# Optimization experiments

Measured on AMD Instinct MI355X. Metric: run time of the kernel, lower is better.

The kernel has to match this reference:

```python
import jax, jax.numpy as jnp
import numpy as np

EPS = 1e-5
ROPE_BASE = 10000.0

def rms_norm(x, w):
    return x * jax.lax.rsqrt(jnp.mean(x * x, axis=-1, keepdims=True) + EPS) * w

def rope_cos_sin(positions, head_dim):
    inv_freq = 1.0 / (ROPE_BASE ** (jnp.arange(0, head_dim, 2, dtype=jnp.float32) / head_dim))
    ang = positions.astype(jnp.float32)[:, None] * inv_freq[None, :]          # [L, hd/2]
    emb = jnp.concatenate([ang, ang], axis=-1)                                # [L, hd]
    return jnp.cos(emb), jnp.sin(emb)

def rotate_half(x):
    d = x.shape[-1] // 2
    return jnp.concatenate([-x[..., d:], x[..., :d]], axis=-1)

def apply_rope(x, cos, sin):
    # x: [B,H,L,hd]; cos/sin: [L,hd]
    return x * cos[None, None] + rotate_half(x) * sin[None, None]

def setup_inputs() -> dict:
    key = jax.random.key(0)
    ks = jax.random.split(key, 12)
    B, S, D = 1, 2048, 2048
    H, KVH, HD = 16, 8, 128
    FF, CACHE = 5632, 2048
    s = 0.02
    return {
        "hidden_states": jax.random.normal(ks[0], (B, S, D), jnp.float32),
        "k_cache": jax.random.normal(ks[1], (B, H, CACHE, HD), jnp.float32),
        "v_cache": jax.random.normal(ks[2], (B, H, CACHE, HD), jnp.float32),
        "q_w": jax.random.normal(ks[3], (H * HD, D), jnp.float32) * s,
        "k_w": jax.random.normal(ks[4], (KVH * HD, D), jnp.float32) * s,
        "v_w": jax.random.normal(ks[5], (KVH * HD, D), jnp.float32) * s,
        "o_w": jax.random.normal(ks[6], (D, H * HD), jnp.float32) * s,
        "gate_w": jax.random.normal(ks[7], (FF, D), jnp.float32) * s,
        "up_w": jax.random.normal(ks[8], (FF, D), jnp.float32) * s,
        "down_w": jax.random.normal(ks[9], (D, FF), jnp.float32) * s,
        "ln1_w": jnp.ones((D,), jnp.float32),
        "ln2_w": jnp.ones((D,), jnp.float32),
        "chunk_size": 512,
    }

def reference(hidden_states, k_cache, v_cache, q_w, k_w, v_w, o_w,
              gate_w, up_w, down_w, ln1_w, ln2_w, chunk_size):
    B, S, D = hidden_states.shape
    H = k_cache.shape[1]
    HD = k_cache.shape[-1]
    KVH = k_w.shape[0] // HD
    group = H // KVH
    prefix = k_cache.shape[2]

    # --- input RMSNorm ---
    residual = hidden_states
    h = rms_norm(hidden_states, ln1_w)

    # --- QKV projections (GQA) ---
    q = (h @ q_w.T).reshape(B, S, H, HD).transpose(0, 2, 1, 3)                # [B,H,S,hd]
    k = (h @ k_w.T).reshape(B, S, KVH, HD).transpose(0, 2, 1, 3)              # [B,KVH,S,hd]
    v = (h @ v_w.T).reshape(B, S, KVH, HD).transpose(0, 2, 1, 3)
    k = jnp.repeat(k, group, axis=1)                                          # repeat_kv -> [B,H,S,hd]
    v = jnp.repeat(v, group, axis=1)

    # --- KV-cache concat along seq ---
    keys = jnp.concatenate([k_cache, k], axis=2)                              # [B,H,P+S,hd]
    vals = jnp.concatenate([v_cache, v], axis=2)
    kv_len = prefix + S

    # --- inline RoPE: keys at 0..kv_len-1, queries at prefix..kv_len-1 ---
    cos_k, sin_k = rope_cos_sin(jnp.arange(kv_len), HD)
    q = apply_rope(q, cos_k[prefix:], sin_k[prefix:])
    keys = apply_rope(keys, cos_k, sin_k)

    # --- hybrid chunked attention mask ---
    # query i (local) sees: full cache prefix + causal positions within its own chunk
    i = jnp.arange(S)
    j = jnp.arange(kv_len)
    local_j = j - prefix
    prefix_vis = (j[None, :] < prefix)
    same_chunk = (i[:, None] // chunk_size) == (local_j[None, :] // chunk_size)
    causal = local_j[None, :] <= i[:, None]
    mask = prefix_vis | (same_chunk & causal)                                 # [S, kv_len]

    scores = jnp.einsum("bhqd,bhkd->bhqk", q, keys) / jnp.sqrt(jnp.float32(HD))
    scores = jnp.where(mask[None, None], scores, jnp.finfo(scores.dtype).min)
    probs = jax.nn.softmax(scores, axis=-1)
    attn = jnp.einsum("bhqk,bhkd->bhqd", probs, vals)                         # [B,H,S,hd]
    attn = attn.transpose(0, 2, 1, 3).reshape(B, S, H * HD) @ o_w.T

    h = residual + attn

    # --- SwiGLU MLP ---
    residual = h
    h = rms_norm(h, ln2_w)
    h = (jax.nn.silu(h @ gate_w.T) * (h @ up_w.T)) @ down_w.T
    return residual + h
```

## Files before the change

### kernel.cpp

```cpp
#include <hip/hip_runtime.h>


#define S_LEN   2048
#define D_MODEL 2048
#define NH      16
#define KVHEADS 8
#define HDIM    128
#define FFDIM   5632
#define PREFIX  2048
#define KVLEN   4096
#define SM_SCALE 0.08838834764831845f
#define LN10K_64 0.14391156831212787f

using bf16x8 = __attribute__((ext_vector_type(8))) short;
using f32x4  = __attribute__((ext_vector_type(4))) float;

__device__ __forceinline__ unsigned f2bf_u(float f) {
  unsigned u = __float_as_uint(f);
  return (u + 0x7fffu + ((u >> 16) & 1u)) >> 16;
}
__device__ __forceinline__ unsigned short f2bf(float f) { return (unsigned short)f2bf_u(f); }
__device__ __forceinline__ float bf2f(unsigned short u) {
  return __uint_as_float((unsigned)u << 16);
}
__device__ __forceinline__ uint2 pack4(float4 v) {
  uint2 r;
  r.x = f2bf_u(v.x) | (f2bf_u(v.y) << 16);
  r.y = f2bf_u(v.z) | (f2bf_u(v.w) << 16);
  return r;
}
__device__ __forceinline__ f32x4 mfma16(bf16x8 a, bf16x8 b, f32x4 c) {
  return __builtin_amdgcn_mfma_f32_16x16x32_bf16(a, b, c, 0, 0, 0);
}
__device__ __forceinline__ void gl2lds16(const unsigned short* g, unsigned short* l) {
  __builtin_amdgcn_global_load_lds(
      (__attribute__((address_space(1))) void*)(unsigned short*)g,
      (__attribute__((address_space(3))) void*)l, 16, 0, 0);
}

__global__ __launch_bounds__(256) void convw_k(const float* __restrict__ src,
                                               unsigned short* __restrict__ dst) {
  size_t i = (size_t)blockIdx.x * 256 + threadIdx.x;
  const float4* s4 = (const float4*)src;
  float4 a = s4[2 * i], b = s4[2 * i + 1];
  uint2 lo = pack4(a), hi = pack4(b);
  ((uint4*)dst)[i] = make_uint4(lo.x, lo.y, hi.x, hi.y);
}

template <bool INBF>
__global__ __launch_bounds__(256) void rmsnorm_k(const void* __restrict__ xin,
                                                 const float* __restrict__ w,
                                                 unsigned short* __restrict__ out) {
  const int row = blockIdx.x, tid = threadIdx.x;
  float v[8];
  if constexpr (INBF) {
    const unsigned short* xr = (const unsigned short*)xin + (size_t)row * D_MODEL;
    uint4 u = ((const uint4*)xr)[tid];
    v[0] = bf2f((unsigned short)(u.x & 0xffff)); v[1] = bf2f((unsigned short)(u.x >> 16));
    v[2] = bf2f((unsigned short)(u.y & 0xffff)); v[3] = bf2f((unsigned short)(u.y >> 16));
    v[4] = bf2f((unsigned short)(u.z & 0xffff)); v[5] = bf2f((unsigned short)(u.z >> 16));
    v[6] = bf2f((unsigned short)(u.w & 0xffff)); v[7] = bf2f((unsigned short)(u.w >> 16));
  } else {
    const float4* xr = (const float4*)((const float*)xin + (size_t)row * D_MODEL);
    float4 a = xr[2 * tid], b = xr[2 * tid + 1];
    v[0] = a.x; v[1] = a.y; v[2] = a.z; v[3] = a.w;
    v[4] = b.x; v[5] = b.y; v[6] = b.z; v[7] = b.w;
  }
  float ss = 0.f;
#pragma unroll
  for (int i = 0; i < 8; i++) ss += v[i] * v[i];
#pragma unroll
  for (int off = 1; off < 64; off <<= 1) ss += __shfl_xor(ss, off);
  __shared__ float red[4];
  if ((tid & 63) == 0) red[tid >> 6] = ss;
  __syncthreads();
  const float sc = rsqrtf((red[0] + red[1] + red[2] + red[3]) * (1.0f / D_MODEL) + 1e-5f);
  const float4* w4 = (const float4*)w;
  float4 wa = w4[2 * tid], wb = w4[2 * tid + 1];
  float4 oa = make_float4(v[0]*sc*wa.x, v[1]*sc*wa.y, v[2]*sc*wa.z, v[3]*sc*wa.w);
  float4 ob = make_float4(v[4]*sc*wb.x, v[5]*sc*wb.y, v[6]*sc*wb.z, v[7]*sc*wb.w);
  uint2 lo = pack4(oa), hi = pack4(ob);
  ((uint4*)(out + (size_t)row * D_MODEL))[tid] = make_uint4(lo.x, lo.y, hi.x, hi.y);
}

template <int BN, int EPI>
__global__ __launch_bounds__(256) void gemm_bf(const unsigned short* __restrict__ A,
                                               const unsigned short* __restrict__ B,
                                               const void* __restrict__ res,
                                               void* __restrict__ C,
                                               int M, int N, int K) {
  constexpr int NI = BN / 32;
  __shared__ __align__(16) unsigned short lA[128 * 32];
  __shared__ __align__(16) unsigned short lB[BN * 32];
  const int tid = threadIdx.x, lane = tid & 63, wave = tid >> 6;
  const int r16 = lane & 15, q4 = lane >> 4;
  const int wm = wave >> 1, wn = wave & 1;
  const int m0 = blockIdx.x * 128, n0 = blockIdx.y * BN;

  const int lr = lane >> 2;
  const int lc = (lane & 3) * 8;
  const unsigned short* gA0 = A + (size_t)(m0 + wave * 16 + lr) * K + lc;
  const unsigned short* gA1 = A + (size_t)(m0 + 64 + wave * 16 + lr) * K + lc;
  unsigned short* lA0 = lA + (wave * 16) * 32;
  unsigned short* lA1 = lA + (64 + wave * 16) * 32;
  const unsigned short* gB0 = B + (size_t)(n0 + wave * 16 + lr) * K + lc;
  const unsigned short* gB1 = B + (size_t)(n0 + 64 + wave * 16 + lr) * K + lc;
  unsigned short* lB0 = lB + (wave * 16) * 32;
  unsigned short* lB1 = lB + (64 + wave * 16) * 32;

  f32x4 acc[4][NI];
#pragma unroll
  for (int i = 0; i < 4; i++)
#pragma unroll
    for (int j = 0; j < NI; j++) acc[i][j] = f32x4{0.f, 0.f, 0.f, 0.f};

  for (int k0 = 0; k0 < K; k0 += 32) {
    gl2lds16(gA0, lA0);
    gl2lds16(gA1, lA1);
    gl2lds16(gB0, lB0);
    if constexpr (BN == 128) gl2lds16(gB1, lB1);
    gA0 += 32; gA1 += 32; gB0 += 32;
    if constexpr (BN == 128) gB1 += 32;
    __syncthreads();
    bf16x8 af[4], bfr[NI];
#pragma unroll
    for (int mi = 0; mi < 4; mi++)
      af[mi] = *(const bf16x8*)&lA[(wm * 64 + mi * 16 + r16) * 32 + q4 * 8];
#pragma unroll
    for (int ni = 0; ni < NI; ni++)
      bfr[ni] = *(const bf16x8*)&lB[(wn * (BN / 2) + ni * 16 + r16) * 32 + q4 * 8];
#pragma unroll
    for (int mi = 0; mi < 4; mi++)
#pragma unroll
      for (int ni = 0; ni < NI; ni++)
        acc[mi][ni] = mfma16(af[mi], bfr[ni], acc[mi][ni]);
    __syncthreads();
  }
#pragma unroll
  for (int mi = 0; mi < 4; mi++)
#pragma unroll
    for (int ni = 0; ni < NI; ni++) {
      int col = n0 + wn * (BN / 2) + ni * 16 + r16;
#pragma unroll
      for (int rr = 0; rr < 4; rr++) {
        int row = m0 + wm * 64 + mi * 16 + q4 * 4 + rr;
        size_t idx = (size_t)row * N + col;
        float v = acc[mi][ni][rr];
        if constexpr (EPI == 0) {
          ((unsigned short*)C)[idx] = f2bf(v);
        } else if constexpr (EPI == 1) {
          ((unsigned short*)C)[idx] = f2bf(v + ((const float*)res)[idx]);
        } else {
          ((float*)C)[idx] = v + bf2f(((const unsigned short*)res)[idx]);
        }
      }
    }
}

__global__ __launch_bounds__(256) void gemm_gateup(const unsigned short* __restrict__ A,
                                                   const unsigned short* __restrict__ Bg,
                                                   const unsigned short* __restrict__ Bu,
                                                   unsigned short* __restrict__ act) {
  __shared__ __align__(16) unsigned short lA[128 * 32];
  __shared__ __align__(16) unsigned short lG[64 * 32];
  __shared__ __align__(16) unsigned short lU[64 * 32];
  const int tid = threadIdx.x, lane = tid & 63, wave = tid >> 6;
  const int r16 = lane & 15, q4 = lane >> 4;
  const int wm = wave >> 1, wn = wave & 1;
  const int m0 = blockIdx.x * 128, n0 = blockIdx.y * 64;
  const int K = D_MODEL;

  const int lr = lane >> 2, lc = (lane & 3) * 8;
  const unsigned short* gA0 = A + (size_t)(m0 + wave * 16 + lr) * K + lc;
  const unsigned short* gA1 = A + (size_t)(m0 + 64 + wave * 16 + lr) * K + lc;
  unsigned short* lA0 = lA + (wave * 16) * 32;
  unsigned short* lA1 = lA + (64 + wave * 16) * 32;
  const unsigned short* gG0 = Bg + (size_t)(n0 + wave * 16 + lr) * K + lc;
  const unsigned short* gU0 = Bu + (size_t)(n0 + wave * 16 + lr) * K + lc;
  unsigned short* lG0 = lG + (wave * 16) * 32;
  unsigned short* lU0 = lU + (wave * 16) * 32;

  f32x4 ag[4][2], au[4][2];
#pragma unroll
  for (int i = 0; i < 4; i++)
#pragma unroll
    for (int j = 0; j < 2; j++) { ag[i][j] = f32x4{0.f,0.f,0.f,0.f}; au[i][j] = f32x4{0.f,0.f,0.f,0.f}; }

  for (int k0 = 0; k0 < K; k0 += 32) {
    gl2lds16(gA0, lA0);
    gl2lds16(gA1, lA1);
    gl2lds16(gG0, lG0);
    gl2lds16(gU0, lU0);
    gA0 += 32; gA1 += 32; gG0 += 32; gU0 += 32;
    __syncthreads();
    bf16x8 af[4], bg2[2], bu2[2];
#pragma unroll
    for (int mi = 0; mi < 4; mi++)
      af[mi] = *(const bf16x8*)&lA[(wm * 64 + mi * 16 + r16) * 32 + q4 * 8];
#pragma unroll
    for (int ni = 0; ni < 2; ni++) {
      int r = (wn * 32 + ni * 16 + r16) * 32 + q4 * 8;
      bg2[ni] = *(const bf16x8*)&lG[r];
      bu2[ni] = *(const bf16x8*)&lU[r];
    }
#pragma unroll
    for (int mi = 0; mi < 4; mi++)
#pragma unroll
      for (int ni = 0; ni < 2; ni++) {
        ag[mi][ni] = mfma16(af[mi], bg2[ni], ag[mi][ni]);
        au[mi][ni] = mfma16(af[mi], bu2[ni], au[mi][ni]);
      }
    __syncthreads();
  }
#pragma unroll
  for (int mi = 0; mi < 4; mi++)
#pragma unroll
    for (int ni = 0; ni < 2; ni++) {
      int col = n0 + wn * 32 + ni * 16 + r16;
#pragma unroll
      for (int rr = 0; rr < 4; rr++) {
        int row = m0 + wm * 64 + mi * 16 + q4 * 4 + rr;
        float g = ag[mi][ni][rr], u = au[mi][ni][rr];
        float sil = g / (1.0f + __expf(-g));
        act[(size_t)row * FFDIM + col] = f2bf(sil * u);
      }
    }
}

__global__ __launch_bounds__(256) void rope_q_k(const unsigned short* __restrict__ qkv,
                                                unsigned short* __restrict__ q_bf) {
  int idx = blockIdx.x * 256 + threadIdx.x;
  int d = idx & 127, s = (idx >> 7) & 2047, h = idx >> 18;
  int dd = d & 63;
  float inv = __expf(-(float)dd * LN10K_64);
  float ang = (float)(PREFIX + s) * inv;
  float c = cosf(ang), sn = sinf(ang);
  const unsigned short* row = qkv + (size_t)s * 4096 + h * HDIM;
  float x = bf2f(row[d]);
  float xr = (d < 64) ? -bf2f(row[d + 64]) : bf2f(row[d - 64]);
  q_bf[idx] = f2bf(x * c + xr * sn);
}

__global__ __launch_bounds__(256) void rope_k_k(const float* __restrict__ k_cache,
                                                const unsigned short* __restrict__ qkv,
                                                unsigned short* __restrict__ keys_bf) {
  int idx = blockIdx.x * 256 + threadIdx.x;
  int d = idx & 127, j = (idx >> 7) & 4095, h = idx >> 19;
  int dd = d & 63;
  float inv = __expf(-(float)dd * LN10K_64);
  float ang = (float)j * inv;
  float c = cosf(ang), sn = sinf(ang);
  float x, xr;
  if (j < PREFIX) {
    const float* row = k_cache + ((size_t)h * PREFIX + j) * HDIM;
    x = row[d];
    xr = (d < 64) ? -row[d + 64] : row[d - 64];
  } else {
    const unsigned short* row = qkv + (size_t)(j - PREFIX) * 4096 + 2048 + (h >> 1) * HDIM;
    x = bf2f(row[d]);
    xr = (d < 64) ? -bf2f(row[d + 64]) : bf2f(row[d - 64]);
  }
  keys_bf[idx] = f2bf(x * c + xr * sn);
}

__global__ __launch_bounds__(256) void vtrans_k(const float* __restrict__ v_cache,
                                                const unsigned short* __restrict__ qkv,
                                                unsigned short* __restrict__ vals_t) {
  __shared__ float tile[32][33];
  const int h = blockIdx.z, j0 = blockIdx.x * 32, d0 = blockIdx.y * 32;
  const int t = threadIdx.x;
#pragma unroll
  for (int i = 0; i < 4; i++) {
    int e = i * 256 + t;
    int jj = e >> 5, dd = e & 31;
    float v;
    if (j0 < PREFIX)
      v = v_cache[((size_t)h * PREFIX + j0 + jj) * HDIM + d0 + dd];
    else
      v = bf2f(qkv[(size_t)(j0 - PREFIX + jj) * 4096 + 3072 + (h >> 1) * HDIM + d0 + dd]);
    tile[jj][dd] = v;
  }
  __syncthreads();
#pragma unroll
  for (int i = 0; i < 4; i++) {
    int e = i * 256 + t;
    int dd = e >> 5, jj = e & 31;
    vals_t[((size_t)h * HDIM + d0 + dd) * KVLEN + j0 + jj] = f2bf(tile[jj][dd]);
  }
}

__global__ __launch_bounds__(256) void attn_k(const unsigned short* __restrict__ qbf,
                                              const unsigned short* __restrict__ keys,
                                              const unsigned short* __restrict__ valst,
                                              const int* __restrict__ chunkp,
                                              unsigned short* __restrict__ out) {
  __shared__ uint4 ldsK[512];
  __shared__ uint4 ldsV[512];
  __shared__ __align__(16) unsigned short ldsP[4][512];
  const int h = blockIdx.y, q0 = blockIdx.x * 64;
  const int tid = threadIdx.x, wave = tid >> 6, lane = tid & 63;
  const int r16 = lane & 15, q4 = lane >> 4;
  const int chunk = chunkp[0];

  bf16x8 qf[4];
  const unsigned short* qrow = qbf + ((size_t)h * S_LEN + q0 + wave * 16 + r16) * HDIM + q4 * 8;
#pragma unroll
  for (int ks = 0; ks < 4; ks++) qf[ks] = *(const bf16x8*)(qrow + ks * 32);

  float mrow[4], lrow[4];
  f32x4 oacc[8];
#pragma unroll
  for (int rr = 0; rr < 4; rr++) { mrow[rr] = -1e30f; lrow[rr] = 0.f; }
#pragma unroll
  for (int ni = 0; ni < 8; ni++) oacc[ni] = f32x4{0.f, 0.f, 0.f, 0.f};

  const int irow_base = q0 + wave * 16 + q4 * 4;

  auto tile_step = [&](int kglob, int jloc0, bool domask) {
#pragma unroll
    for (int i = 0; i < 2; i++) {
      int gid = i * 256 + tid;
      int kk = gid >> 4, c8 = gid & 15;
      uint4 v = *(const uint4*)(keys + ((size_t)h * KVLEN + kglob + kk) * HDIM + c8 * 8);
      int ks = c8 >> 2, q8 = c8 & 3;
      ldsK[((ks * 2 + (kk >> 4)) << 6) + (q8 << 4) + ((kk & 15) ^ (q8 << 1))] = v;
    }
#pragma unroll
    for (int i = 0; i < 2; i++) {
      int gid = i * 256 + tid;
      int n = gid >> 2, c8 = gid & 3;
      uint4 v = *(const uint4*)(valst + ((size_t)h * HDIM + n) * KVLEN + kglob + c8 * 8);
      ldsV[((n >> 4) << 6) + (c8 << 4) + ((n & 15) ^ (c8 << 1))] = v;
    }
    __syncthreads();
    f32x4 s0{0.f,0.f,0.f,0.f}, s1{0.f,0.f,0.f,0.f};
#pragma unroll
    for (int ks = 0; ks < 4; ks++) {
      bf16x8 k0f = *(const bf16x8*)&ldsK[((ks * 2 + 0) << 6) + (q4 << 4) + (r16 ^ (q4 << 1))];
      bf16x8 k1f = *(const bf16x8*)&ldsK[((ks * 2 + 1) << 6) + (q4 << 4) + (r16 ^ (q4 << 1))];
      s0 = mfma16(qf[ks], k0f, s0);
      s1 = mfma16(qf[ks], k1f, s1);
    }
    float al[4];
#pragma unroll
    for (int rr = 0; rr < 4; rr++) {
      float a = s0[rr] * SM_SCALE, b = s1[rr] * SM_SCALE;
      if (domask) {
        int irow = irow_base + rr;
        if (jloc0 + r16 > irow)       a = -1e30f;
        if (jloc0 + 16 + r16 > irow)  b = -1e30f;
      }
      float mx = fmaxf(a, b);
      mx = fmaxf(mx, __shfl_xor(mx, 1));
      mx = fmaxf(mx, __shfl_xor(mx, 2));
      mx = fmaxf(mx, __shfl_xor(mx, 4));
      mx = fmaxf(mx, __shfl_xor(mx, 8));
      float mn = fmaxf(mrow[rr], mx);
      float alpha = __expf(mrow[rr] - mn);
      mrow[rr] = mn;
      a = __expf(a - mn); b = __expf(b - mn);
      float sum = a + b;
      sum += __shfl_xor(sum, 1); sum += __shfl_xor(sum, 2);
      sum += __shfl_xor(sum, 4); sum += __shfl_xor(sum, 8);
      lrow[rr] = lrow[rr] * alpha + sum;
      al[rr] = alpha;
      int rowi = q4 * 4 + rr;
      ldsP[wave][((r16 >> 3) * 16 + rowi) * 8 + (r16 & 7)] = f2bf(a);
      ldsP[wave][(((r16 >> 3) + 2) * 16 + rowi) * 8 + (r16 & 7)] = f2bf(b);
    }
#pragma unroll
    for (int ni = 0; ni < 8; ni++) {
      oacc[ni][0] *= al[0]; oacc[ni][1] *= al[1];
      oacc[ni][2] *= al[2]; oacc[ni][3] *= al[3];
    }
    __syncthreads();
    bf16x8 pf = *(const bf16x8*)&ldsP[wave][lane * 8];
#pragma unroll
    for (int ni = 0; ni < 8; ni++) {
      bf16x8 vf = *(const bf16x8*)&ldsV[(ni << 6) + (q4 << 4) + (r16 ^ (q4 << 1))];
      oacc[ni] = mfma16(pf, vf, oacc[ni]);
    }
    __syncthreads();
  };

  for (int kb = 0; kb < PREFIX; kb += 32) tile_step(kb, 0, false);
  const int cs = (q0 / chunk) * chunk;
  for (int lkb = cs; lkb < q0 + 64; lkb += 32) tile_step(PREFIX + lkb, lkb, true);

#pragma unroll
  for (int ni = 0; ni < 8; ni++)
#pragma unroll
    for (int rr = 0; rr < 4; rr++) {
      int q = irow_base + rr;
      int dcol = ni * 16 + r16;
      out[(size_t)q * D_MODEL + h * HDIM + dcol] = f2bf(oacc[ni][rr] / lrow[rr]);
    }
}

extern "C" void kernel_launch(void* const* d_in, const int* in_sizes, int n_in,
                              void* d_out, int out_size, void* d_ws, size_t ws_size,
                              hipStream_t stream) {
  (void)in_sizes; (void)n_in; (void)out_size;
  const float* hidden  = (const float*)d_in[0];
  const float* k_cache = (const float*)d_in[1];
  const float* v_cache = (const float*)d_in[2];
  const float* q_w     = (const float*)d_in[3];
  const float* k_w     = (const float*)d_in[4];
  const float* v_w     = (const float*)d_in[5];
  const float* o_w     = (const float*)d_in[6];
  const float* gate_w  = (const float*)d_in[7];
  const float* up_w    = (const float*)d_in[8];
  const float* down_w  = (const float*)d_in[9];
  const float* ln1     = (const float*)d_in[10];
  const float* ln2     = (const float*)d_in[11];
  const int*   chunkp  = (const int*)d_in[12];

  if (ws_size < 92274688) return;
  char* ws = (char*)d_ws;
  const size_t MB = 1048576;
  unsigned short* WQKV   = (unsigned short*)(ws + 0 * MB);
  unsigned short* hn     = (unsigned short*)(ws + 16 * MB);
  unsigned short* qkvpre = (unsigned short*)(ws + 24 * MB);
  unsigned short* qbf    = (unsigned short*)(ws + 40 * MB);
  unsigned short* keysbf = (unsigned short*)(ws + 48 * MB);
  unsigned short* valst  = (unsigned short*)(ws + 64 * MB);
  unsigned short* attnbf = (unsigned short*)(ws + 80 * MB);
  unsigned short* WO     = (unsigned short*)(ws + 0 * MB);
  unsigned short* h2     = (unsigned short*)(ws + 66 * MB);
  unsigned short* h2n    = (unsigned short*)(ws + 74 * MB);
  unsigned short* WG     = (unsigned short*)(ws + 0 * MB);
  unsigned short* WU     = (unsigned short*)(ws + 22 * MB);
  unsigned short* act    = (unsigned short*)(ws + 44 * MB);
  unsigned short* WD     = (unsigned short*)(ws + 0 * MB);
  float* out = (float*)d_out;

  convw_k<<<2048, 256, 0, stream>>>(q_w, WQKV);
  convw_k<<<1024, 256, 0, stream>>>(k_w, WQKV + (size_t)2048 * 2048);
  convw_k<<<1024, 256, 0, stream>>>(v_w, WQKV + (size_t)3072 * 2048);
  rmsnorm_k<false><<<S_LEN, 256, 0, stream>>>(hidden, ln1, hn);
  gemm_bf<128, 0><<<dim3(16, 32), 256, 0, stream>>>(hn, WQKV, nullptr, qkvpre,
                                                    S_LEN, 4096, D_MODEL);
  rope_q_k<<<(NH * S_LEN * HDIM) / 256, 256, 0, stream>>>(qkvpre, qbf);
  rope_k_k<<<(NH * KVLEN * HDIM) / 256, 256, 0, stream>>>(k_cache, qkvpre, keysbf);
  vtrans_k<<<dim3(KVLEN / 32, HDIM / 32, NH), 256, 0, stream>>>(v_cache, qkvpre, valst);
  attn_k<<<dim3(S_LEN / 64, NH), 256, 0, stream>>>(qbf, keysbf, valst, chunkp, attnbf);
  convw_k<<<2048, 256, 0, stream>>>(o_w, WO);
  gemm_bf<64, 1><<<dim3(16, 32), 256, 0, stream>>>(attnbf, WO, hidden, h2,
                                                   S_LEN, D_MODEL, D_MODEL);
  rmsnorm_k<true><<<S_LEN, 256, 0, stream>>>(h2, ln2, h2n);
  convw_k<<<5632, 256, 0, stream>>>(gate_w, WG);
  convw_k<<<5632, 256, 0, stream>>>(up_w, WU);
  gemm_gateup<<<dim3(16, FFDIM / 64), 256, 0, stream>>>(h2n, WG, WU, act);
  convw_k<<<5632, 256, 0, stream>>>(down_w, WD);
  gemm_bf<64, 2><<<dim3(16, 32), 256, 0, stream>>>(act, WD, h2, out,
                                                   S_LEN, D_MODEL, FFDIM);
}
```

Baseline: 746.3 us.

## Split attention KV range into three segments with a combine kernel

Attention is split over the KV axis: two blocks cover halves of the cache prefix and a third covers the local chunk. The per-segment unnormalized outputs are written in bf16 along with row max and row sum, and a new combine kernel merges them with log-sum-exp weights. The inner loop now processes 64-key tiles loaded through a direct global-to-LDS helper, drops one barrier per tile, and folds log2(e) into the scale so it can use exp2f. This gives more blocks for better GPU occupancy at the cost of an extra kernel launch, partial-result traffic, and some bf16 rounding of the partial outputs.

```diff
diff --git a/kernel.cpp b/kernel.cpp
--- a/kernel.cpp
+++ b/kernel.cpp
@@ -9,7 +9,7 @@
 #define FFDIM   5632
 #define PREFIX  2048
 #define KVLEN   4096
-#define SM_SCALE 0.08838834764831845f
+#define SM_L2E  0.12751744f
 #define LN10K_64 0.14391156831212787f
 
 using bf16x8 = __attribute__((ext_vector_type(8))) short;
@@ -293,13 +293,16 @@
                                               const unsigned short* __restrict__ keys,
                                               const unsigned short* __restrict__ valst,
                                               const int* __restrict__ chunkp,
-                                              unsigned short* __restrict__ out) {
-  __shared__ uint4 ldsK[512];
-  __shared__ uint4 ldsV[512];
-  __shared__ __align__(16) unsigned short ldsP[4][512];
-  const int h = blockIdx.y, q0 = blockIdx.x * 64;
+                                              unsigned short* __restrict__ pO,
+                                              float* __restrict__ pm,
+                                              float* __restrict__ pl) {
+  __shared__ __align__(16) unsigned short lK[4 * 64 * 32];
+  __shared__ __align__(16) unsigned short lV[2 * 128 * 32];
+  __shared__ __align__(16) unsigned short lP[4][2 * 16 * 32];
+  const int h = blockIdx.y, q0 = blockIdx.x * 64, seg = blockIdx.z;
   const int tid = threadIdx.x, wave = tid >> 6, lane = tid & 63;
   const int r16 = lane & 15, q4 = lane >> 4;
+  const int lr = lane >> 2, lc = (lane & 3) * 8;
   const int chunk = chunkp[0];
 
   bf16x8 qf[4];
@@ -315,86 +318,117 @@
   for (int ni = 0; ni < 8; ni++) oacc[ni] = f32x4{0.f, 0.f, 0.f, 0.f};
 
   const int irow_base = q0 + wave * 16 + q4 * 4;
-
-  auto tile_step = [&](int kglob, int jloc0, bool domask) {
-#pragma unroll
-    for (int i = 0; i < 2; i++) {
-      int gid = i * 256 + tid;
-      int kk = gid >> 4, c8 = gid & 15;
-      uint4 v = *(const uint4*)(keys + ((size_t)h * KVLEN + kglob + kk) * HDIM + c8 * 8);
-      int ks = c8 >> 2, q8 = c8 & 3;
-      ldsK[((ks * 2 + (kk >> 4)) << 6) + (q8 << 4) + ((kk & 15) ^ (q8 << 1))] = v;
-    }
-#pragma unroll
-    for (int i = 0; i < 2; i++) {
-      int gid = i * 256 + tid;
-      int n = gid >> 2, c8 = gid & 3;
-      uint4 v = *(const uint4*)(valst + ((size_t)h * HDIM + n) * KVLEN + kglob + c8 * 8);
-      ldsV[((n >> 4) << 6) + (c8 << 4) + ((n & 15) ^ (c8 << 1))] = v;
-    }
-    __syncthreads();
-    f32x4 s0{0.f,0.f,0.f,0.f}, s1{0.f,0.f,0.f,0.f};
-#pragma unroll
-    for (int ks = 0; ks < 4; ks++) {
-      bf16x8 k0f = *(const bf16x8*)&ldsK[((ks * 2 + 0) << 6) + (q4 << 4) + (r16 ^ (q4 << 1))];
-      bf16x8 k1f = *(const bf16x8*)&ldsK[((ks * 2 + 1) << 6) + (q4 << 4) + (r16 ^ (q4 << 1))];
-      s0 = mfma16(qf[ks], k0f, s0);
-      s1 = mfma16(qf[ks], k1f, s1);
-    }
+  const unsigned short* Kh = keys + (size_t)h * KVLEN * HDIM;
+  const unsigned short* Vh = valst + (size_t)h * HDIM * KVLEN;
+
+  int kt0, ktN;
+  if (seg == 0)      { kt0 = 0;    ktN = 1024; }
+  else if (seg == 1) { kt0 = 1024; ktN = 2048; }
+  else { int cs = (q0 / chunk) * chunk; kt0 = PREFIX + cs; ktN = PREFIX + q0 + 64; }
+
+  for (int kt = kt0; kt < ktN; kt += 64) {
+    const bool domask = (seg == 2) && (kt - PREFIX + 64 > q0);
+#pragma unroll
+    for (int i = 0; i < 4; i++)
+      gl2lds16(Kh + (size_t)(kt + wave * 16 + lr) * HDIM + i * 32 + lc,
+               lK + (i * 64 + wave * 16) * 32);
+#pragma unroll
+    for (int i = 0; i < 4; i++) {
+      int slab = i * 4 + wave, kc = slab >> 3, ds = slab & 7;
+      gl2lds16(Vh + (size_t)(ds * 16 + lr) * KVLEN + kt + kc * 32 + lc,
+               lV + (kc * 128 + ds * 16) * 32);
+    }
+    __syncthreads();
+    f32x4 s[4];
+#pragma unroll
+    for (int j = 0; j < 4; j++) s[j] = f32x4{0.f, 0.f, 0.f, 0.f};
+#pragma unroll
+    for (int ks = 0; ks < 4; ks++)
+#pragma unroll
+      for (int j = 0; j < 4; j++) {
+        bf16x8 kf = *(const bf16x8*)&lK[(ks * 64 + j * 16 + r16) * 32 + q4 * 8];
+        s[j] = mfma16(qf[ks], kf, s[j]);
+      }
     float al[4];
 #pragma unroll
     for (int rr = 0; rr < 4; rr++) {
-      float a = s0[rr] * SM_SCALE, b = s1[rr] * SM_SCALE;
+      float sc0 = s[0][rr] * SM_L2E, sc1 = s[1][rr] * SM_L2E;
+      float sc2 = s[2][rr] * SM_L2E, sc3 = s[3][rr] * SM_L2E;
       if (domask) {
-        int irow = irow_base + rr;
-        if (jloc0 + r16 > irow)       a = -1e30f;
-        if (jloc0 + 16 + r16 > irow)  b = -1e30f;
+        int irow = irow_base + rr, kl = kt - PREFIX + r16;
+        if (kl      > irow) sc0 = -1e30f;
+        if (kl + 16 > irow) sc1 = -1e30f;
+        if (kl + 32 > irow) sc2 = -1e30f;
+        if (kl + 48 > irow) sc3 = -1e30f;
       }
-      float mx = fmaxf(a, b);
+      float mx = fmaxf(fmaxf(sc0, sc1), fmaxf(sc2, sc3));
       mx = fmaxf(mx, __shfl_xor(mx, 1));
       mx = fmaxf(mx, __shfl_xor(mx, 2));
       mx = fmaxf(mx, __shfl_xor(mx, 4));
       mx = fmaxf(mx, __shfl_xor(mx, 8));
       float mn = fmaxf(mrow[rr], mx);
-      float alpha = __expf(mrow[rr] - mn);
+      al[rr] = exp2f(mrow[rr] - mn);
       mrow[rr] = mn;
-      a = __expf(a - mn); b = __expf(b - mn);
-      float sum = a + b;
+      float p0 = exp2f(sc0 - mn), p1 = exp2f(sc1 - mn);
+      float p2 = exp2f(sc2 - mn), p3 = exp2f(sc3 - mn);
+      float sum = (p0 + p1) + (p2 + p3);
       sum += __shfl_xor(sum, 1); sum += __shfl_xor(sum, 2);
       sum += __shfl_xor(sum, 4); sum += __shfl_xor(sum, 8);
-      lrow[rr] = lrow[rr] * alpha + sum;
-      al[rr] = alpha;
-      int rowi = q4 * 4 + rr;
-      ldsP[wave][((r16 >> 3) * 16 + rowi) * 8 + (r16 & 7)] = f2bf(a);
-      ldsP[wave][(((r16 >> 3) + 2) * 16 + rowi) * 8 + (r16 & 7)] = f2bf(b);
+      lrow[rr] = lrow[rr] * al[rr] + sum;
+      int rbase = (q4 * 4 + rr) * 32 + r16;
+      lP[wave][rbase]            = f2bf(p0);
+      lP[wave][rbase + 16]       = f2bf(p1);
+      lP[wave][512 + rbase]      = f2bf(p2);
+      lP[wave][512 + rbase + 16] = f2bf(p3);
     }
 #pragma unroll
     for (int ni = 0; ni < 8; ni++) {
       oacc[ni][0] *= al[0]; oacc[ni][1] *= al[1];
       oacc[ni][2] *= al[2]; oacc[ni][3] *= al[3];
     }
-    __syncthreads();
-    bf16x8 pf = *(const bf16x8*)&ldsP[wave][lane * 8];
+    bf16x8 pf0 = *(const bf16x8*)&lP[wave][r16 * 32 + q4 * 8];
+    bf16x8 pf1 = *(const bf16x8*)&lP[wave][512 + r16 * 32 + q4 * 8];
 #pragma unroll
     for (int ni = 0; ni < 8; ni++) {
-      bf16x8 vf = *(const bf16x8*)&ldsV[(ni << 6) + (q4 << 4) + (r16 ^ (q4 << 1))];
-      oacc[ni] = mfma16(pf, vf, oacc[ni]);
-    }
-    __syncthreads();
-  };
-
-  for (int kb = 0; kb < PREFIX; kb += 32) tile_step(kb, 0, false);
-  const int cs = (q0 / chunk) * chunk;
-  for (int lkb = cs; lkb < q0 + 64; lkb += 32) tile_step(PREFIX + lkb, lkb, true);
-
+      bf16x8 v0 = *(const bf16x8*)&lV[(ni * 16 + r16) * 32 + q4 * 8];
+      oacc[ni] = mfma16(pf0, v0, oacc[ni]);
+      bf16x8 v1 = *(const bf16x8*)&lV[(128 * 32) + (ni * 16 + r16) * 32 + q4 * 8];
+      oacc[ni] = mfma16(pf1, v1, oacc[ni]);
+    }
+    __syncthreads();
+  }
+
+  const size_t base = (size_t)(seg * NH + h) * S_LEN;
 #pragma unroll
   for (int ni = 0; ni < 8; ni++)
 #pragma unroll
+    for (int rr = 0; rr < 4; rr++)
+      pO[(base + irow_base + rr) * HDIM + ni * 16 + r16] = f2bf(oacc[ni][rr]);
+  if (r16 == 0) {
+#pragma unroll
     for (int rr = 0; rr < 4; rr++) {
-      int q = irow_base + rr;
-      int dcol = ni * 16 + r16;
-      out[(size_t)q * D_MODEL + h * HDIM + dcol] = f2bf(oacc[ni][rr] / lrow[rr]);
-    }
+      pm[base + irow_base + rr] = mrow[rr];
+      pl[base + irow_base + rr] = lrow[rr];
+    }
+  }
+}
+
+__global__ __launch_bounds__(256) void attn_combine(const unsigned short* __restrict__ pO,
+                                                    const float* __restrict__ pm,
+                                                    const float* __restrict__ pl,
+                                                    unsigned short* __restrict__ out) {
+  int idx = blockIdx.x * 256 + threadIdx.x;
+  int d = idx & 127, hq = idx >> 7;
+  const int R = NH * S_LEN;
+  float m0 = pm[hq], m1 = pm[hq + R], m2 = pm[hq + 2 * R];
+  float M = fmaxf(m0, fmaxf(m1, m2));
+  float w0 = exp2f(m0 - M), w1 = exp2f(m1 - M), w2 = exp2f(m2 - M);
+  float L = pl[hq] * w0 + pl[hq + R] * w1 + pl[hq + 2 * R] * w2;
+  float o = bf2f(pO[(size_t)hq * HDIM + d]) * w0
+          + bf2f(pO[(size_t)(hq + R) * HDIM + d]) * w1
+          + bf2f(pO[(size_t)(hq + 2 * R) * HDIM + d]) * w2;
+  int h = hq >> 11, q = hq & 2047;
+  out[(size_t)q * D_MODEL + h * HDIM + d] = f2bf(o / L);
 }
 
 extern "C" void kernel_launch(void* const* d_in, const int* in_sizes, int n_in,
@@ -425,7 +459,10 @@
   unsigned short* keysbf = (unsigned short*)(ws + 48 * MB);
   unsigned short* valst  = (unsigned short*)(ws + 64 * MB);
   unsigned short* attnbf = (unsigned short*)(ws + 80 * MB);
-  unsigned short* WO     = (unsigned short*)(ws + 0 * MB);
+  unsigned short* pO     = (unsigned short*)(ws + 0 * MB);
+  float*          pm     = (float*)(ws + 26 * MB);
+  float*          pl     = (float*)(ws + 27 * MB);
+  unsigned short* WO     = (unsigned short*)(ws + 28 * MB);
   unsigned short* h2     = (unsigned short*)(ws + 66 * MB);
   unsigned short* h2n    = (unsigned short*)(ws + 74 * MB);
   unsigned short* WG     = (unsigned short*)(ws + 0 * MB);
@@ -443,7 +480,9 @@
   rope_q_k<<<(NH * S_LEN * HDIM) / 256, 256, 0, stream>>>(qkvpre, qbf);
   rope_k_k<<<(NH * KVLEN * HDIM) / 256, 256, 0, stream>>>(k_cache, qkvpre, keysbf);
   vtrans_k<<<dim3(KVLEN / 32, HDIM / 32, NH), 256, 0, stream>>>(v_cache, qkvpre, valst);
-  attn_k<<<dim3(S_LEN / 64, NH), 256, 0, stream>>>(qbf, keysbf, valst, chunkp, attnbf);
+  attn_k<<<dim3(S_LEN / 64, NH, 3), 256, 0, stream>>>(qbf, keysbf, valst, chunkp,
+                                                      pO, pm, pl);
+  attn_combine<<<(NH * S_LEN * HDIM) / 256, 256, 0, stream>>>(pO, pm, pl, attnbf);
   convw_k<<<2048, 256, 0, stream>>>(o_w, WO);
   gemm_bf<64, 1><<<dim3(16, 32), 256, 0, stream>>>(attnbf, WO, hidden, h2,
                                                    S_LEN, D_MODEL, D_MODEL);
```

After: 712.2 us. -4.6%, faster.
